# Performance work log

Hardware: AMD Instinct MI355X
Metric: run time of the kernel (lower is better)

The kernel has to match this reference:

```python
import jax, jax.numpy as jnp
import numpy as np

NUM_CODES = 4096
EMBED_DIM = 64
BETA = 0.25


def setup_inputs() -> dict:
    key = jax.random.key(0)
    k1, k2 = jax.random.split(key)
    z = jax.random.normal(k1, (8, EMBED_DIM, 64, 64), dtype=jnp.float32)
    weight = jax.random.normal(k2, (NUM_CODES, EMBED_DIM), dtype=jnp.float32)
    return {"z": z, "weight": weight}


def reference(z, weight):
    # z: [B, C, H, W] -> [B, H, W, C]
    z_bhwc = jnp.moveaxis(z, 1, -1)
    z_flat = z_bhwc.reshape(-1, EMBED_DIM)  # [N, d]

    # squared-euclidean distances: ||z||^2 + ||w||^2 - 2 z.w  -> [N, num_codes]
    distance = (
        jnp.sum(z_flat ** 2, axis=1, keepdims=True)
        + jnp.sum(weight ** 2, axis=1)
        - 2.0 * jnp.einsum('bd,nd->bn', z_flat, weight)
    )
    encoding_indices = jnp.argmin(distance, axis=1)  # [N]

    # codebook lookup (gather)
    z_q = weight[encoding_indices].reshape(z_bhwc.shape)  # [B, H, W, C]

    encodings = jax.nn.one_hot(encoding_indices, NUM_CODES, dtype=z.dtype)  # [N, num_codes]
    avg_probs = jnp.mean(encodings, axis=0)
    tiny = 1e-10  # max(1e-10, finfo(fp32).tiny)
    perplexity = jnp.exp(-jnp.sum(avg_probs * jnp.log(avg_probs + tiny)))

    # commitment loss (z_q detached) — eval path, no EMA state update
    loss = BETA * jnp.mean((jax.lax.stop_gradient(z_q) - z_bhwc) ** 2)

    # straight-through estimator
    z_q = z_bhwc + jax.lax.stop_gradient(z_q - z_bhwc)
    z_q = jnp.moveaxis(z_q, -1, 1)  # back to [B, C, H, W]

    return z_q, loss, perplexity, encodings, encoding_indices
```

## Files before the change

### kernel.cpp

```cpp
#include <hip/hip_runtime.h>
#include <math.h>
#include <float.h>

#define ZQ_OFF   0
#define LOSS_OFF 2097152
#define PERP_OFF 2097153
#define ENC_OFF  2097154
#define IDX_OFF  136314882ULL
#define BETA     0.25f


__global__ void vq_wnorm(const float* __restrict__ w, float* __restrict__ wnorm) {
    int c = blockIdx.x * 256 + threadIdx.x;
    const float4* w4 = (const float4*)(w + ((size_t)c << 6));
    float s = 0.f;
    #pragma unroll
    for (int k = 0; k < 16; ++k) { float4 v = w4[k]; s += v.x*v.x + v.y*v.y + v.z*v.z + v.w*v.w; }
    wnorm[c] = s;
}

__global__ __launch_bounds__(256, 2) void vq_main(
    const float* __restrict__ z, const float* __restrict__ w,
    const float* __restrict__ wnorm, float* __restrict__ out,
    float* __restrict__ loss_ws, int* __restrict__ ticket, int* __restrict__ hist)
{
    __shared__ float zT[64][64];
    __shared__ float wl[128 * 65];
    __shared__ int   s_widx[64];
    __shared__ int   s_flag;

    const int tx   = threadIdx.x;
    const int tcol = tx & 31;
    const int trow = tx >> 5;
    const int base = blockIdx.x * 64;
    const int bb   = base >> 12;
    const int hh   = (base & 4095) >> 6;

    #pragma unroll
    for (int j = 0; j < 4; ++j) {
        int f4 = j * 256 + tx;
        int d  = f4 >> 4, k = f4 & 15;
        float4 v = *(const float4*)(z + (((size_t)bb * 64 + d) * 64 + hh) * 64 + k * 4);
        *(float4*)&zT[d][k * 4] = v;
    }

    float best[8]; int bidx[8];
    #pragma unroll
    for (int i = 0; i < 8; ++i) { best[i] = FLT_MAX; bidx[i] = 0; }

    float* enc = out + ENC_OFF;

    for (int ch = 0; ch < 32; ++ch) {
        const int cbase = ch << 7;
        __syncthreads();

        #pragma unroll
        for (int j = 0; j < 8; ++j) {
            int f4 = j * 256 + tx;
            int c  = f4 >> 4, k = f4 & 15;
            float4 v = *(const float4*)(w + ((size_t)(cbase + c) << 6) + k * 4);
            float* p = &wl[c * 65 + k * 4];
            p[0] = v.x; p[1] = v.y; p[2] = v.z; p[3] = v.w;
        }
        float wn0 = wnorm[cbase + tcol];
        float wn1 = wnorm[cbase + tcol + 32];
        float wn2 = wnorm[cbase + tcol + 64];
        float wn3 = wnorm[cbase + tcol + 96];
        #pragma unroll
        for (int j = 0; j < 16; ++j) {
            int f2 = (ch << 12) + j * 256 + tx;
            int r  = f2 >> 11, c2 = f2 & 2047;
            *((float2*)(enc + ((size_t)(base + r) << 12)) + c2) = make_float2(0.f, 0.f);
        }
        __syncthreads();

        float acc[8][4];
        #pragma unroll
        for (int i = 0; i < 8; ++i)
            { acc[i][0] = 0.f; acc[i][1] = 0.f; acc[i][2] = 0.f; acc[i][3] = 0.f; }

        #pragma unroll 4
        for (int d = 0; d < 64; ++d) {
            float4 za = *(const float4*)&zT[d][trow * 8];
            float4 zb = *(const float4*)&zT[d][trow * 8 + 4];
            float zr0[8] = { za.x, za.y, za.z, za.w, zb.x, zb.y, zb.z, zb.w };
            float wv[4];
            wv[0] = wl[(tcol      ) * 65 + d];
            wv[1] = wl[(tcol + 32 ) * 65 + d];
            wv[2] = wl[(tcol + 64 ) * 65 + d];
            wv[3] = wl[(tcol + 96 ) * 65 + d];
            #pragma unroll
            for (int i = 0; i < 8; ++i)
                #pragma unroll
                for (int j = 0; j < 4; ++j)
                    acc[i][j] = fmaf(zr0[i], wv[j], acc[i][j]);
        }

        #pragma unroll
        for (int i = 0; i < 8; ++i) {
            float s0 = fmaf(-2.f, acc[i][0], wn0);
            if (s0 < best[i]) { best[i] = s0; bidx[i] = cbase + tcol; }
            float s1 = fmaf(-2.f, acc[i][1], wn1);
            if (s1 < best[i]) { best[i] = s1; bidx[i] = cbase + tcol + 32; }
            float s2 = fmaf(-2.f, acc[i][2], wn2);
            if (s2 < best[i]) { best[i] = s2; bidx[i] = cbase + tcol + 64; }
            float s3 = fmaf(-2.f, acc[i][3], wn3);
            if (s3 < best[i]) { best[i] = s3; bidx[i] = cbase + tcol + 96; }
        }
    }

    __syncthreads();
    float2* red = (float2*)wl;
    #pragma unroll
    for (int i = 0; i < 8; ++i)
        red[(trow * 8 + i) * 32 + tcol] = make_float2(best[i], __int_as_float(bidx[i]));
    __syncthreads();

    if (tx < 64) {
        float b = FLT_MAX; int bi = 0x7fffffff;
        for (int c = 0; c < 32; ++c) {
            float2 v = red[tx * 32 + c];
            int vi = __float_as_int(v.y);
            if (v.x < b || (v.x == b && vi < bi)) { b = v.x; bi = vi; }
        }
        s_widx[tx] = bi;
        out[IDX_OFF + (size_t)(base + tx)] = (float)bi;
        atomicAdd(&hist[bi], 1);
        enc[((size_t)(base + tx) << 12) + bi] = 1.0f;
    }
    __syncthreads();

    {
        const int row = tx & 63;
        const int dg  = tx >> 6;
        const int wi  = s_widx[row];
        const float* qrow = w + ((size_t)wi << 6);
        float lsum = 0.f;
        #pragma unroll
        for (int dd = 0; dd < 16; ++dd) {
            int d = dg * 16 + dd;
            float q  = qrow[d];
            float zv = zT[d][row];
            float diff = q - zv;
            lsum += diff * diff;
            out[ZQ_OFF + (((size_t)bb * 64 + d) * 64 + hh) * 64 + row] = zv + (q - zv);
        }
        #pragma unroll
        for (int off = 32; off > 0; off >>= 1) lsum += __shfl_down(lsum, off, 64);
        if ((tx & 63) == 0) atomicAdd(loss_ws, lsum);
    }

    __syncthreads();
    if (tx == 0) {
        __threadfence();
        int old = atomicAdd(ticket, 1);
        s_flag = (old == 511) ? 1 : 0;
    }
    __syncthreads();
    if (s_flag) {
        __threadfence();
        float s = 0.f;
        #pragma unroll
        for (int j = 0; j < 16; ++j) {
            int c = tx + j * 256;
            int cnt = atomicAdd(&hist[c], 0);
            float p = (float)cnt * (1.f / 32768.f);
            s += p * logf(p + 1e-10f);
        }
        float* fr = wl;
        fr[tx] = s;
        __syncthreads();
        for (int off = 128; off > 0; off >>= 1) {
            if (tx < off) fr[tx] += fr[tx + off];
            __syncthreads();
        }
        if (tx == 0) {
            out[LOSS_OFF] = BETA * atomicAdd(loss_ws, 0.f) / 2097152.f;
            out[PERP_OFF] = expf(-fr[0]);
        }
    }
}

extern "C" void kernel_launch(void* const* d_in, const int* in_sizes, int n_in,
                              void* d_out, int out_size, void* d_ws, size_t ws_size,
                              hipStream_t stream)
{
    const float* z = (const float*)d_in[0];
    const float* w = (const float*)d_in[1];
    float* out     = (float*)d_out;
    float* loss_ws = (float*)d_ws;
    int*   ticket  = (int*)((char*)d_ws + 4);
    int*   hist    = (int*)((char*)d_ws + 16);
    float* wnorm   = (float*)((char*)d_ws + 16400);

    hipMemsetAsync(d_ws, 0, 16 + 4096 * sizeof(int), stream);
    vq_wnorm<<<16, 256, 0, stream>>>(w, wnorm);
    vq_main<<<512, 256, 0, stream>>>(z, w, wnorm, out, loss_ws, ticket, hist);
}
```

Baseline: 742.8 us.

## Enlarge register tile to 8x8 codes per thread with float4 LDS loads

Each chunk now covers 256 codes instead of 128, and each thread accumulates an 8x8 register tile. The codebook is staged in two 32-wide slices of the embedding dimension with a 36-float padded stride, so the inner loop can read float4 vectors from LDS instead of scalar loads. This raises FMAs per LDS load and halves the number of chunks. The cost is higher register pressure from 64 accumulators plus staged vectors, which may cause spills or lower occupancy under launch_bounds(256,2).

```diff
diff --git a/kernel.cpp b/kernel.cpp
--- a/kernel.cpp
+++ b/kernel.cpp
@@ -24,8 +24,8 @@
     const float* __restrict__ wnorm, float* __restrict__ out,
     float* __restrict__ loss_ws, int* __restrict__ ticket, int* __restrict__ hist)
 {
-    __shared__ float zT[64][64];
-    __shared__ float wl[128 * 65];
+    __shared__ float zD[64][64];
+    __shared__ float wl[256 * 36];
     __shared__ int   s_widx[64];
     __shared__ int   s_flag;
 
@@ -39,9 +39,9 @@
     #pragma unroll
     for (int j = 0; j < 4; ++j) {
         int f4 = j * 256 + tx;
-        int d  = f4 >> 4, k = f4 & 15;
-        float4 v = *(const float4*)(z + (((size_t)bb * 64 + d) * 64 + hh) * 64 + k * 4);
-        *(float4*)&zT[d][k * 4] = v;
+        int d  = f4 >> 4, w4i = f4 & 15;
+        float4 v = *(const float4*)(z + (((size_t)bb * 64 + d) * 64 + hh) * 64 + w4i * 4);
+        *(float4*)&zD[d][w4i * 4] = v;
     }
 
     float best[8]; int bidx[8];
@@ -50,62 +50,75 @@
 
     float* enc = out + ENC_OFF;
 
-    for (int ch = 0; ch < 32; ++ch) {
-        const int cbase = ch << 7;
-        __syncthreads();
-
-        #pragma unroll
-        for (int j = 0; j < 8; ++j) {
-            int f4 = j * 256 + tx;
-            int c  = f4 >> 4, k = f4 & 15;
-            float4 v = *(const float4*)(w + ((size_t)(cbase + c) << 6) + k * 4);
-            float* p = &wl[c * 65 + k * 4];
-            p[0] = v.x; p[1] = v.y; p[2] = v.z; p[3] = v.w;
-        }
-        float wn0 = wnorm[cbase + tcol];
-        float wn1 = wnorm[cbase + tcol + 32];
-        float wn2 = wnorm[cbase + tcol + 64];
-        float wn3 = wnorm[cbase + tcol + 96];
-        #pragma unroll
-        for (int j = 0; j < 16; ++j) {
-            int f2 = (ch << 12) + j * 256 + tx;
-            int r  = f2 >> 11, c2 = f2 & 2047;
-            *((float2*)(enc + ((size_t)(base + r) << 12)) + c2) = make_float2(0.f, 0.f);
-        }
-        __syncthreads();
-
-        float acc[8][4];
+    for (int ch = 0; ch < 16; ++ch) {
+        const int cbase = ch << 8;
+        float wn[8];
+        #pragma unroll
+        for (int k = 0; k < 8; ++k) wn[k] = wnorm[cbase + tcol + 32 * k];
+
+        float acc[8][8];
         #pragma unroll
         for (int i = 0; i < 8; ++i)
-            { acc[i][0] = 0.f; acc[i][1] = 0.f; acc[i][2] = 0.f; acc[i][3] = 0.f; }
-
-        #pragma unroll 4
-        for (int d = 0; d < 64; ++d) {
-            float4 za = *(const float4*)&zT[d][trow * 8];
-            float4 zb = *(const float4*)&zT[d][trow * 8 + 4];
-            float zr0[8] = { za.x, za.y, za.z, za.w, zb.x, zb.y, zb.z, zb.w };
-            float wv[4];
-            wv[0] = wl[(tcol      ) * 65 + d];
-            wv[1] = wl[(tcol + 32 ) * 65 + d];
-            wv[2] = wl[(tcol + 64 ) * 65 + d];
-            wv[3] = wl[(tcol + 96 ) * 65 + d];
-            #pragma unroll
-            for (int i = 0; i < 8; ++i)
+            #pragma unroll
+            for (int k = 0; k < 8; ++k) acc[i][k] = 0.f;
+
+        #pragma unroll
+        for (int s = 0; s < 2; ++s) {
+            __syncthreads();
+            #pragma unroll
+            for (int j = 0; j < 8; ++j) {
+                int f4 = j * 256 + tx;
+                int c  = f4 >> 3, q = f4 & 7;
+                float4 v = ((const float4*)w)[(size_t)(cbase + c) * 16 + s * 8 + q];
+                *(float4*)&wl[c * 36 + q * 4] = v;
+            }
+            #pragma unroll
+            for (int j = 0; j < 16; ++j) {
+                int f2 = ((ch * 2 + s) * 16 + j) * 256 + tx;
+                int r  = f2 >> 11, c2 = f2 & 2047;
+                *((float2*)(enc + ((size_t)(base + r) << 12)) + c2) = make_float2(0.f, 0.f);
+            }
+            __syncthreads();
+
+            #pragma unroll
+            for (int dg = 0; dg < 8; ++dg) {
+                const int d0 = s * 32 + dg * 4;
+                float4 zv0[4], zv1[4];
                 #pragma unroll
-                for (int j = 0; j < 4; ++j)
-                    acc[i][j] = fmaf(zr0[i], wv[j], acc[i][j]);
+                for (int e = 0; e < 4; ++e) {
+                    zv0[e] = *(const float4*)&zD[d0 + e][trow * 8];
+                    zv1[e] = *(const float4*)&zD[d0 + e][trow * 8 + 4];
+                }
+                float4 wv[8];
+                #pragma unroll
+                for (int k = 0; k < 8; ++k)
+                    wv[k] = *(const float4*)&wl[(tcol + 32 * k) * 36 + dg * 4];
+                #pragma unroll
+                for (int k = 0; k < 8; ++k) {
+                    #pragma unroll
+                    for (int e = 0; e < 4; ++e) {
+                        const float wf = (e == 0) ? wv[k].x : (e == 1) ? wv[k].y
+                                        : (e == 2) ? wv[k].z : wv[k].w;
+                        acc[0][k] = fmaf(zv0[e].x, wf, acc[0][k]);
+                        acc[1][k] = fmaf(zv0[e].y, wf, acc[1][k]);
+                        acc[2][k] = fmaf(zv0[e].z, wf, acc[2][k]);
+                        acc[3][k] = fmaf(zv0[e].w, wf, acc[3][k]);
+                        acc[4][k] = fmaf(zv1[e].x, wf, acc[4][k]);
+                        acc[5][k] = fmaf(zv1[e].y, wf, acc[5][k]);
+                        acc[6][k] = fmaf(zv1[e].z, wf, acc[6][k]);
+                        acc[7][k] = fmaf(zv1[e].w, wf, acc[7][k]);
+                    }
+                }
+            }
         }
 
         #pragma unroll
         for (int i = 0; i < 8; ++i) {
-            float s0 = fmaf(-2.f, acc[i][0], wn0);
-            if (s0 < best[i]) { best[i] = s0; bidx[i] = cbase + tcol; }
-            float s1 = fmaf(-2.f, acc[i][1], wn1);
-            if (s1 < best[i]) { best[i] = s1; bidx[i] = cbase + tcol + 32; }
-            float s2 = fmaf(-2.f, acc[i][2], wn2);
-            if (s2 < best[i]) { best[i] = s2; bidx[i] = cbase + tcol + 64; }
-            float s3 = fmaf(-2.f, acc[i][3], wn3);
-            if (s3 < best[i]) { best[i] = s3; bidx[i] = cbase + tcol + 96; }
+            #pragma unroll
+            for (int k = 0; k < 8; ++k) {
+                float sc = fmaf(-2.f, acc[i][k], wn[k]);
+                if (sc < best[i]) { best[i] = sc; bidx[i] = cbase + tcol + 32 * k; }
+            }
         }
     }
 
@@ -140,7 +153,7 @@
         for (int dd = 0; dd < 16; ++dd) {
             int d = dg * 16 + dd;
             float q  = qrow[d];
-            float zv = zT[d][row];
+            float zv = zD[d][row];
             float diff = q - zv;
             lsum += diff * diff;
             out[ZQ_OFF + (((size_t)bb * 64 + d) * 64 + hh) * 64 + row] = zv + (q - zv);
```

After: 742.2 us. About the same (-0.1%).
